# Performance work log

Hardware: AMD Instinct MI355X
Metric: run time of the kernel (lower is better)

Reference implementation:

```python
import jax, jax.numpy as jnp
import numpy as np

THRESH = 0.4


def setup_inputs() -> dict:
    key = jax.random.key(0)
    ks = jax.random.split(key, 8)
    B, N, C, H, O = 8, 16384, 640, 256, 128
    s = 0.02  # small init so sigmoid(logits) ~ 0.5 -> realistic mixed selection
    return {
        "point_features": jax.random.normal(ks[0], (B, N, C), jnp.float32),
        "point_coords": jax.random.normal(ks[1], (B, N, 3), jnp.float32) * 10.0,
        "w1": jax.random.normal(ks[2], (C, H), jnp.float32) * s,
        "b1": jnp.zeros((H,), jnp.float32),
        "w2": jax.random.normal(ks[3], (H, 1), jnp.float32) * s,
        "b2": jnp.zeros((1,), jnp.float32),
        "wo": jax.random.normal(ks[4], (C, O), jnp.float32) * s,
        "bo": jnp.zeros((O,), jnp.float32),
    }


def reference(point_features, point_coords, w1, b1, w2, b2, wo, bo):
    B, N, _ = point_features.shape
    # 2-layer MLP -> per-point logit -> sigmoid score
    h = jax.nn.relu(jnp.einsum('bnc,ch->bnh', point_features, w1) + b1)
    logits = jnp.einsum('bnh,ho->bno', h, w2) + b2          # [B, N, 1]
    scores = jax.nn.sigmoid(logits)                          # [B, N, 1]
    # score-scaled features through output projection
    feats = jnp.einsum('bnc,co->bno', point_features * scores, wo) + bo  # [B, N, O]
    # score-threshold selection + per-batch stream compaction into a
    # zero-padded tensor (padded to N, the jit-static worst case)
    sel = scores[..., 0] > THRESH                            # [B, N] bool
    pos = jnp.cumsum(sel.astype(jnp.int32), axis=1) - 1      # destination slot
    pos = jnp.where(sel, pos, N)                             # unselected -> OOB (dropped)
    bidx = jnp.arange(B)[:, None]
    selected_keypoints = jnp.zeros_like(feats).at[bidx, pos].set(feats, mode='drop')
    selected_coords = jnp.zeros_like(point_coords).at[bidx, pos].set(point_coords, mode='drop')
    # point_mask: True where the row is zero padding (matches (coords==0).sum(-1)!=0)
    point_mask = jnp.sum(selected_coords == 0, axis=-1) != 0
    return selected_keypoints, selected_coords, point_mask
```

## Files before the change

kernel.cpp:

```cpp
#include <hip/hip_runtime.h>
#include <hip/hip_bf16.h>


typedef __attribute__((ext_vector_type(8))) short short8v;
typedef __attribute__((ext_vector_type(4))) float f32x4;

#define M_TOTAL 131072
#define C_DIM 640
#define H_DIM 256
#define O_DIM 128
#define NCOMB 384
#define TM 64
#define KSTEPS 20
#define N_PTS 16384
#define TILES_PER_B 256
#define NTILES 2048
#define THRL -0.4054651081f
#define FIX_MARGIN 0.03f

#define OUT_COORD_OFF 16777216
#define OUT_MASK_OFF  17170432

#define WT_OFF     0u
#define TMASK_OFF  491520u
#define TAGG_OFF   507904u
#define TEXCL_OFF  516096u
#define COUNTS_OFF 524288u
#define G_OFF      1572864u

__device__ __forceinline__ int swzA(int u) {
  return u ^ (((u >> 3) & 1) | (((u >> 6) & 3) << 1));
}
__device__ __forceinline__ int swzB(int u) { return u ^ ((u >> 3) & 7); }

__device__ __forceinline__ void glds16(const void* g, void* l) {
  const __attribute__((address_space(1))) unsigned int* gp =
      reinterpret_cast<const __attribute__((address_space(1))) unsigned int*>(
          reinterpret_cast<uintptr_t>(g));
  __attribute__((address_space(3))) unsigned int* lp =
      reinterpret_cast<__attribute__((address_space(3))) unsigned int*>(
          reinterpret_cast<uintptr_t>(l));
  __builtin_amdgcn_global_load_lds(gp, lp, 16, 0, 0);
}

__device__ __forceinline__ unsigned int f2bf_bits(float f) {
  unsigned int u = __builtin_bit_cast(unsigned int, f);
  return (u + 0x7fffu + ((u >> 16) & 1u)) >> 16;
}
__device__ __forceinline__ unsigned int pack_bf2(float lo, float hi) {
  return f2bf_bits(lo) | (f2bf_bits(hi) << 16);
}

__global__ __launch_bounds__(256) void convert_w(const float* __restrict__ w1,
                                                 const float* __restrict__ wo,
                                                 unsigned short* __restrict__ Wt2) {
  int o = blockIdx.x * 256 + threadIdx.x;
  if (o < NCOMB * C_DIM) {
    int e = o & 7;
    int chunk = o >> 3;
    int ks = chunk / 1536;
    int r = chunk - ks * 1536;
    int u = swzB(r);
    int n = u >> 2, kg = u & 3;
    int k = ks * 32 + kg * 8 + e;
    float v = (n < H_DIM) ? w1[k * H_DIM + n] : wo[k * O_DIM + (n - H_DIM)];
    Wt2[o] = (unsigned short)f2bf_bits(v);
  }
}

__global__ __launch_bounds__(512, 4) void gemm_fused(
    const float* __restrict__ pf, const unsigned short* __restrict__ Wt2,
    const float* __restrict__ w1, const float* __restrict__ b1,
    const float* __restrict__ w2, const float* __restrict__ b2,
    const float* __restrict__ bo, unsigned long long* __restrict__ tmask,
    int* __restrict__ tagg, float* __restrict__ G) {
  __shared__ __align__(16) unsigned short As[2][256 * 8];
  __shared__ __align__(16) unsigned short Bs[2][1536 * 8];
  __shared__ float lpart[8][64];
  __shared__ float llog[64];
  __shared__ float srow[64];
  __shared__ unsigned long long s_fixmask;

  const int tid = threadIdx.x;
  const int lane = tid & 63;
  const int wv = tid >> 6;
  const int q = lane & 15;
  const int p = lane >> 4;
  const int tile = blockIdx.x;
  const int m0 = tile * TM;

  f32x4 acc[3][4];
#pragma unroll
  for (int i = 0; i < 3; ++i)
#pragma unroll
    for (int rt = 0; rt < 4; ++rt) acc[i][rt] = (f32x4){0.f, 0.f, 0.f, 0.f};

  const int ar = tid >> 3;
  const int ah = tid & 7;
  const float* asrc = pf + (size_t)(m0 + ar) * C_DIM + ah * 4;
  const int awp = swzA(((ah >> 1) << 6) + ar) * 8 + (ah & 1) * 4;

  float4 rB;
  {
    float4 rA = *(const float4*)(asrc);
    rB = *(const float4*)(asrc + 32);
#pragma unroll
    for (int u = 0; u < 3; ++u)
      glds16(Wt2 + (size_t)(u * 512 + tid) * 8, &Bs[0][(u * 512 + tid) * 8]);
    *(uint2*)&As[0][awp] = make_uint2(pack_bf2(rA.x, rA.y), pack_bf2(rA.z, rA.w));
    __syncthreads();
  }

#pragma unroll 2
  for (int t = 0; t < KSTEPS; ++t) {
    const int cur = t & 1;
    float4 rC;
    if (t + 2 < KSTEPS) rC = *(const float4*)(asrc + (t + 2) * 32);
    if (t + 1 < KSTEPS) {
#pragma unroll
      for (int u = 0; u < 3; ++u)
        glds16(Wt2 + (size_t)((t + 1) * 1536 + u * 512 + tid) * 8,
               &Bs[cur ^ 1][(u * 512 + tid) * 8]);
    }
    short8v af[4];
#pragma unroll
    for (int rt = 0; rt < 4; ++rt)
      af[rt] = *(const short8v*)&As[cur][swzA((p << 6) + rt * 16 + q) * 8];
#pragma unroll
    for (int i = 0; i < 3; ++i) {
      const int ub = (((wv + 8 * i) * 16 + q) << 2) + p;
      short8v bfv = *(const short8v*)&Bs[cur][swzB(ub) * 8];
#pragma unroll
      for (int rt = 0; rt < 4; ++rt)
        acc[i][rt] = __builtin_amdgcn_mfma_f32_16x16x32_bf16(af[rt], bfv, acc[i][rt], 0, 0, 0);
    }
    if (t + 1 < KSTEPS)
      *(uint2*)&As[cur ^ 1][awp] = make_uint2(pack_bf2(rB.x, rB.y), pack_bf2(rB.z, rB.w));
    rB = rC;
    __syncthreads();
  }

  float w2v[2], b1v[2];
#pragma unroll
  for (int i = 0; i < 2; ++i) {
    int col = (wv + 8 * i) * 16 + q;
    w2v[i] = w2[col];
    b1v[i] = b1[col];
  }
#pragma unroll
  for (int rt = 0; rt < 4; ++rt) {
    float pr[4] = {0.f, 0.f, 0.f, 0.f};
#pragma unroll
    for (int i = 0; i < 2; ++i)
#pragma unroll
      for (int r = 0; r < 4; ++r)
        pr[r] += fmaxf(acc[i][rt][r] + b1v[i], 0.f) * w2v[i];
#pragma unroll
    for (int mk = 1; mk < 16; mk <<= 1)
#pragma unroll
      for (int r = 0; r < 4; ++r) pr[r] += __shfl_xor(pr[r], mk);
    if (q == 0)
#pragma unroll
      for (int r = 0; r < 4; ++r) lpart[wv][rt * 16 + p * 4 + r] = pr[r];
  }
  __syncthreads();

  bool nf = false;
  if (wv == 0) {
    float lg = b2[0];
#pragma unroll
    for (int w = 0; w < 8; ++w) lg += lpart[w][tid];
    llog[tid] = lg;
    nf = fabsf(lg - THRL) < FIX_MARGIN;
  }
  unsigned long long fm = __ballot(nf);
  if (tid == 0) s_fixmask = fm;
  __syncthreads();

  unsigned long long fixmask = s_fixmask;
  while (fixmask) {
    int row = __ffsll(fixmask) - 1;
    fixmask &= fixmask - 1;
    if (tid < 256) {
      const float* prow = pf + (size_t)(m0 + row) * C_DIM;
      float a0 = 0.f, a1 = 0.f;
      for (int c = 0; c < C_DIM; c += 2) {
        a0 = fmaf(prow[c], w1[(size_t)c * H_DIM + tid], a0);
        a1 = fmaf(prow[c + 1], w1[(size_t)(c + 1) * H_DIM + tid], a1);
      }
      float v = fmaxf(a0 + a1 + b1[tid], 0.f) * w2[tid];
#pragma unroll
      for (int mk = 1; mk < 64; mk <<= 1) v += __shfl_xor(v, mk);
      if (lane == 0) lpart[0][wv] = v;
    }
    __syncthreads();
    if (tid == 0)
      llog[row] = lpart[0][0] + lpart[0][1] + lpart[0][2] + lpart[0][3] + b2[0];
    __syncthreads();
  }

  bool sel = false;
  float flog = 0.f;
  if (wv == 0) {
    flog = llog[tid];
    sel = flog > THRL;
  }
  unsigned long long selmask = __ballot(sel);
  if (wv == 0) {
    srow[tid] = 1.f / (1.f + expf(-flog));
    if (tid == 0) {
      tmask[tile] = selmask;
      tagg[tile] = __popcll(selmask);
    }
  }
  __syncthreads();

  {
    const int gcol = wv * 16 + q;
    const float bov = bo[gcol];
#pragma unroll
    for (int rt = 0; rt < 4; ++rt)
#pragma unroll
      for (int r = 0; r < 4; ++r) {
        int row = rt * 16 + p * 4 + r;
        G[(size_t)(m0 + row) * O_DIM + gcol] = fmaf(acc[2][rt][r], srow[row], bov);
      }
  }
}

__global__ __launch_bounds__(256) void scan_tiles(const int* __restrict__ tagg,
                                                  int* __restrict__ texcl,
                                                  int* __restrict__ counts) {
  __shared__ int wsum[4];
  const int c = blockIdx.x, t = threadIdx.x;
  const int lane = t & 63, w = t >> 6;
  int v = tagg[c * 256 + t];
  int inc = v;
#pragma unroll
  for (int d = 1; d < 64; d <<= 1) {
    int n = __shfl_up(inc, d);
    if (lane >= d) inc += n;
  }
  if (lane == 63) wsum[w] = inc;
  __syncthreads();
  int base = 0;
#pragma unroll
  for (int ww = 0; ww < 4; ++ww)
    if (ww < w) base += wsum[ww];
  texcl[c * 256 + t] = base + inc - v;
  if (t == 255) counts[c] = base + inc;
}

__global__ __launch_bounds__(512) void scatter(
    const float* __restrict__ G, const unsigned long long* __restrict__ tmask,
    const int* __restrict__ texcl, const float* __restrict__ pc,
    float* __restrict__ out) {
  const int tile = blockIdx.x;
  const int tid = threadIdx.x;
  const int lane = tid & 63;
  const int wv = tid >> 6;
  const unsigned long long mask = tmask[tile];
  const int base = (tile >> 8) * N_PTS + texcl[tile];
  const int m0 = tile * TM;
#pragma unroll
  for (int j = 0; j < 8; ++j) {
    const int row = wv * 8 + j;
    if (!((mask >> row) & 1ull)) continue;
    const int dst = base + __popcll(mask & ((1ull << row) - 1ull));
    const int m = m0 + row;
    float2 g = *(const float2*)(G + (size_t)m * O_DIM + lane * 2);
    *(float2*)(out + (size_t)dst * O_DIM + lane * 2) = g;
    if (lane == 0) {
      float c0 = pc[m * 3], c1 = pc[m * 3 + 1], c2 = pc[m * 3 + 2];
      float* oc = out + OUT_COORD_OFF;
      oc[dst * 3] = c0; oc[dst * 3 + 1] = c1; oc[dst * 3 + 2] = c2;
      out[OUT_MASK_OFF + dst] = (c0 == 0.f || c1 == 0.f || c2 == 0.f) ? 1.f : 0.f;
    }
  }
}

__global__ __launch_bounds__(256) void fill_tail(const int* __restrict__ counts,
                                                 float* __restrict__ out) {
  int m = blockIdx.x * 4 + (threadIdx.x >> 6);
  int lane = threadIdx.x & 63;
  int b = m >> 14, j = m & (N_PTS - 1);
  if (j < counts[b]) return;
  *(float2*)(out + (size_t)m * O_DIM + lane * 2) = make_float2(0.f, 0.f);
  if (lane == 0) {
    float* oc = out + OUT_COORD_OFF;
    oc[m * 3] = 0.f; oc[m * 3 + 1] = 0.f; oc[m * 3 + 2] = 0.f;
    out[OUT_MASK_OFF + m] = 1.f;
  }
}

extern "C" void kernel_launch(void* const* d_in, const int* in_sizes, int n_in,
                              void* d_out, int out_size, void* d_ws, size_t ws_size,
                              hipStream_t stream) {
  const float* pf = (const float*)d_in[0];
  const float* pc = (const float*)d_in[1];
  const float* w1 = (const float*)d_in[2];
  const float* b1 = (const float*)d_in[3];
  const float* w2 = (const float*)d_in[4];
  const float* b2 = (const float*)d_in[5];
  const float* wo = (const float*)d_in[6];
  const float* bo = (const float*)d_in[7];
  float* out = (float*)d_out;
  char* ws = (char*)d_ws;

  unsigned short* Wt2 = (unsigned short*)(ws + WT_OFF);
  unsigned long long* tmask = (unsigned long long*)(ws + TMASK_OFF);
  int* tagg = (int*)(ws + TAGG_OFF);
  int* texcl = (int*)(ws + TEXCL_OFF);
  int* counts = (int*)(ws + COUNTS_OFF);
  float* G = (float*)(ws + G_OFF);

  convert_w<<<960, 256, 0, stream>>>(w1, wo, Wt2);
  gemm_fused<<<NTILES, 512, 0, stream>>>(pf, Wt2, w1, b1, w2, b2, bo,
                                         tmask, tagg, G);
  scan_tiles<<<8, 256, 0, stream>>>(tagg, texcl, counts);
  scatter<<<NTILES, 512, 0, stream>>>(G, tmask, texcl, pc, out);
  fill_tail<<<M_TOTAL / 4, 256, 0, stream>>>(counts, out);
}
```

Measured before the change: 200.4 us.

## Double GEMM row tile to 128 with 2x4 warp layout for weight reuse

Grows the fused GEMM tile from 64 to 128 rows and reorganizes the 8 warps into 2 row groups by 4 column groups, each computing 6 column tiles. Each LDS-staged weight tile is reused across twice as many rows, which halves weight loads and barrier overhead per row. In exchange the accumulator count doubles, the occupancy hint drops from 4 to 3, and the tile count halves. The scan and scatter kernels are adapted to use two 64-bit selection masks per tile.

```diff
diff --git a/kernel.cpp b/kernel.cpp
--- a/kernel.cpp
+++ b/kernel.cpp
@@ -10,11 +10,11 @@
 #define H_DIM 256
 #define O_DIM 128
 #define NCOMB 384
-#define TM 64
+#define TM 128
 #define KSTEPS 20
 #define N_PTS 16384
-#define TILES_PER_B 256
-#define NTILES 2048
+#define TILES_PER_B 128
+#define NTILES 1024
 #define THRL -0.4054651081f
 #define FIX_MARGIN 0.03f
 
@@ -24,12 +24,12 @@
 #define WT_OFF     0u
 #define TMASK_OFF  491520u
 #define TAGG_OFF   507904u
-#define TEXCL_OFF  516096u
-#define COUNTS_OFF 524288u
+#define TEXCL_OFF  512000u
+#define COUNTS_OFF 516096u
 #define G_OFF      1572864u
 
-__device__ __forceinline__ int swzA(int u) {
-  return u ^ (((u >> 3) & 1) | (((u >> 6) & 3) << 1));
+__device__ __forceinline__ int swzA2(int u) {
+  return u ^ (((u >> 3) & 1) | (((u >> 7) & 3) << 1));
 }
 __device__ __forceinline__ int swzB(int u) { return u ^ ((u >> 3) & 7); }
 
@@ -68,54 +68,64 @@
   }
 }
 
-__global__ __launch_bounds__(512, 4) void gemm_fused(
+__global__ __launch_bounds__(512, 3) void gemm_fused(
     const float* __restrict__ pf, const unsigned short* __restrict__ Wt2,
     const float* __restrict__ w1, const float* __restrict__ b1,
     const float* __restrict__ w2, const float* __restrict__ b2,
     const float* __restrict__ bo, unsigned long long* __restrict__ tmask,
     int* __restrict__ tagg, float* __restrict__ G) {
-  __shared__ __align__(16) unsigned short As[2][256 * 8];
+  __shared__ __align__(16) unsigned short As[2][512 * 8];
   __shared__ __align__(16) unsigned short Bs[2][1536 * 8];
-  __shared__ float lpart[8][64];
-  __shared__ float llog[64];
-  __shared__ float srow[64];
-  __shared__ unsigned long long s_fixmask;
+  __shared__ float lpart[3][128];
+  __shared__ float llog[128];
+  __shared__ float srow[128];
+  __shared__ float fsum[4];
+  __shared__ unsigned long long s_fm[2];
+  __shared__ unsigned long long s_msk[2];
 
   const int tid = threadIdx.x;
   const int lane = tid & 63;
   const int wv = tid >> 6;
   const int q = lane & 15;
   const int p = lane >> 4;
+  const int wr = wv & 1;
+  const int wc = wv >> 1;
   const int tile = blockIdx.x;
   const int m0 = tile * TM;
 
-  f32x4 acc[3][4];
-#pragma unroll
-  for (int i = 0; i < 3; ++i)
+  f32x4 acc[6][4];
+#pragma unroll
+  for (int i = 0; i < 6; ++i)
 #pragma unroll
     for (int rt = 0; rt < 4; ++rt) acc[i][rt] = (f32x4){0.f, 0.f, 0.f, 0.f};
 
-  const int ar = tid >> 3;
-  const int ah = tid & 7;
-  const float* asrc = pf + (size_t)(m0 + ar) * C_DIM + ah * 4;
-  const int awp = swzA(((ah >> 1) << 6) + ar) * 8 + (ah & 1) * 4;
-
-  float4 rB;
+  const int arow = tid >> 2;
+  const int akg = tid & 3;
+  const float* asrc = pf + (size_t)(m0 + arow) * C_DIM + akg * 8;
+  const int awp = swzA2(akg * 128 + arow) * 8;
+
+  float4 rB0, rB1;
   {
-    float4 rA = *(const float4*)(asrc);
-    rB = *(const float4*)(asrc + 32);
+    float4 a0 = *(const float4*)(asrc);
+    float4 a1 = *(const float4*)(asrc + 4);
 #pragma unroll
     for (int u = 0; u < 3; ++u)
       glds16(Wt2 + (size_t)(u * 512 + tid) * 8, &Bs[0][(u * 512 + tid) * 8]);
-    *(uint2*)&As[0][awp] = make_uint2(pack_bf2(rA.x, rA.y), pack_bf2(rA.z, rA.w));
+    *(uint4*)&As[0][awp] = make_uint4(pack_bf2(a0.x, a0.y), pack_bf2(a0.z, a0.w),
+                                      pack_bf2(a1.x, a1.y), pack_bf2(a1.z, a1.w));
+    rB0 = *(const float4*)(asrc + 32);
+    rB1 = *(const float4*)(asrc + 36);
     __syncthreads();
   }
 
 #pragma unroll 2
   for (int t = 0; t < KSTEPS; ++t) {
     const int cur = t & 1;
-    float4 rC;
-    if (t + 2 < KSTEPS) rC = *(const float4*)(asrc + (t + 2) * 32);
+    float4 rC0 = rB0, rC1 = rB1;
+    if (t + 2 < KSTEPS) {
+      rC0 = *(const float4*)(asrc + (t + 2) * 32);
+      rC1 = *(const float4*)(asrc + (t + 2) * 32 + 4);
+    }
     if (t + 1 < KSTEPS) {
 #pragma unroll
       for (int u = 0; u < 3; ++u)
@@ -125,130 +135,142 @@
     short8v af[4];
 #pragma unroll
     for (int rt = 0; rt < 4; ++rt)
-      af[rt] = *(const short8v*)&As[cur][swzA((p << 6) + rt * 16 + q) * 8];
-#pragma unroll
-    for (int i = 0; i < 3; ++i) {
-      const int ub = (((wv + 8 * i) * 16 + q) << 2) + p;
+      af[rt] = *(const short8v*)&As[cur][swzA2(p * 128 + wr * 64 + rt * 16 + q) * 8];
+#pragma unroll
+    for (int i = 0; i < 6; ++i) {
+      const int ub = (((wc * 6 + i) * 16 + q) << 2) + p;
       short8v bfv = *(const short8v*)&Bs[cur][swzB(ub) * 8];
 #pragma unroll
       for (int rt = 0; rt < 4; ++rt)
         acc[i][rt] = __builtin_amdgcn_mfma_f32_16x16x32_bf16(af[rt], bfv, acc[i][rt], 0, 0, 0);
     }
     if (t + 1 < KSTEPS)
-      *(uint2*)&As[cur ^ 1][awp] = make_uint2(pack_bf2(rB.x, rB.y), pack_bf2(rB.z, rB.w));
-    rB = rC;
+      *(uint4*)&As[cur ^ 1][awp] = make_uint4(pack_bf2(rB0.x, rB0.y), pack_bf2(rB0.z, rB0.w),
+                                              pack_bf2(rB1.x, rB1.y), pack_bf2(rB1.z, rB1.w));
+    rB0 = rC0; rB1 = rC1;
     __syncthreads();
   }
 
-  float w2v[2], b1v[2];
-#pragma unroll
-  for (int i = 0; i < 2; ++i) {
-    int col = (wv + 8 * i) * 16 + q;
-    w2v[i] = w2[col];
-    b1v[i] = b1[col];
-  }
-#pragma unroll
-  for (int rt = 0; rt < 4; ++rt) {
-    float pr[4] = {0.f, 0.f, 0.f, 0.f};
-#pragma unroll
-    for (int i = 0; i < 2; ++i)
-#pragma unroll
-      for (int r = 0; r < 4; ++r)
-        pr[r] += fmaxf(acc[i][rt][r] + b1v[i], 0.f) * w2v[i];
-#pragma unroll
-    for (int mk = 1; mk < 16; mk <<= 1)
-#pragma unroll
-      for (int r = 0; r < 4; ++r) pr[r] += __shfl_xor(pr[r], mk);
-    if (q == 0)
-#pragma unroll
-      for (int r = 0; r < 4; ++r) lpart[wv][rt * 16 + p * 4 + r] = pr[r];
+  if (wc < 3) {
+    float b1v[6], w2v[6];
+#pragma unroll
+    for (int i = 0; i < 6; ++i) {
+      int ct = wc * 6 + i;
+      if (ct < 16) {
+        int col = ct * 16 + q;
+        b1v[i] = b1[col];
+        w2v[i] = w2[col];
+      } else {
+        b1v[i] = 0.f;
+        w2v[i] = 0.f;
+      }
+    }
+#pragma unroll
+    for (int rt = 0; rt < 4; ++rt) {
+      float pr[4] = {0.f, 0.f, 0.f, 0.f};
+#pragma unroll
+      for (int i = 0; i < 6; ++i) {
+        if (wc * 6 + i < 16) {
+#pragma unroll
+          for (int r = 0; r < 4; ++r)
+            pr[r] += fmaxf(acc[i][rt][r] + b1v[i], 0.f) * w2v[i];
+        }
+      }
+#pragma unroll
+      for (int mk = 1; mk < 16; mk <<= 1)
+#pragma unroll
+        for (int r = 0; r < 4; ++r) pr[r] += __shfl_xor(pr[r], mk);
+      if (q == 0)
+#pragma unroll
+        for (int r = 0; r < 4; ++r)
+          lpart[wc][wr * 64 + rt * 16 + p * 4 + r] = pr[r];
+    }
   }
   __syncthreads();
 
-  bool nf = false;
-  if (wv == 0) {
-    float lg = b2[0];
-#pragma unroll
-    for (int w = 0; w < 8; ++w) lg += lpart[w][tid];
+  if (tid < 128) {
+    float lg = lpart[0][tid] + lpart[1][tid] + lpart[2][tid] + b2[0];
     llog[tid] = lg;
-    nf = fabsf(lg - THRL) < FIX_MARGIN;
-  }
-  unsigned long long fm = __ballot(nf);
-  if (tid == 0) s_fixmask = fm;
+    bool nf = fabsf(lg - THRL) < FIX_MARGIN;
+    unsigned long long fm = __ballot(nf);
+    if (lane == 0) s_fm[wv] = fm;
+  }
   __syncthreads();
 
-  unsigned long long fixmask = s_fixmask;
-  while (fixmask) {
-    int row = __ffsll(fixmask) - 1;
-    fixmask &= fixmask - 1;
-    if (tid < 256) {
-      const float* prow = pf + (size_t)(m0 + row) * C_DIM;
-      float a0 = 0.f, a1 = 0.f;
-      for (int c = 0; c < C_DIM; c += 2) {
-        a0 = fmaf(prow[c], w1[(size_t)c * H_DIM + tid], a0);
-        a1 = fmaf(prow[c + 1], w1[(size_t)(c + 1) * H_DIM + tid], a1);
+#pragma unroll 1
+  for (int h = 0; h < 2; ++h) {
+    unsigned long long fixmask = s_fm[h];
+    while (fixmask) {
+      int row = h * 64 + (__ffsll(fixmask) - 1);
+      fixmask &= fixmask - 1;
+      if (tid < 256) {
+        const float* prow = pf + (size_t)(m0 + row) * C_DIM;
+        float a0 = 0.f, a1 = 0.f;
+        for (int c = 0; c < C_DIM; c += 2) {
+          a0 = fmaf(prow[c], w1[(size_t)c * H_DIM + tid], a0);
+          a1 = fmaf(prow[c + 1], w1[(size_t)(c + 1) * H_DIM + tid], a1);
+        }
+        float v = fmaxf(a0 + a1 + b1[tid], 0.f) * w2[tid];
+#pragma unroll
+        for (int mk = 1; mk < 64; mk <<= 1) v += __shfl_xor(v, mk);
+        if (lane == 0) fsum[wv] = v;
       }
-      float v = fmaxf(a0 + a1 + b1[tid], 0.f) * w2[tid];
-#pragma unroll
-      for (int mk = 1; mk < 64; mk <<= 1) v += __shfl_xor(v, mk);
-      if (lane == 0) lpart[0][wv] = v;
-    }
-    __syncthreads();
-    if (tid == 0)
-      llog[row] = lpart[0][0] + lpart[0][1] + lpart[0][2] + lpart[0][3] + b2[0];
-    __syncthreads();
-  }
-
-  bool sel = false;
-  float flog = 0.f;
-  if (wv == 0) {
-    flog = llog[tid];
-    sel = flog > THRL;
-  }
-  unsigned long long selmask = __ballot(sel);
-  if (wv == 0) {
+      __syncthreads();
+      if (tid == 0)
+        llog[row] = fsum[0] + fsum[1] + fsum[2] + fsum[3] + b2[0];
+      __syncthreads();
+    }
+  }
+
+  if (tid < 128) {
+    float flog = llog[tid];
+    bool sel = flog > THRL;
+    unsigned long long mk = __ballot(sel);
     srow[tid] = 1.f / (1.f + expf(-flog));
-    if (tid == 0) {
-      tmask[tile] = selmask;
-      tagg[tile] = __popcll(selmask);
-    }
+    if (lane == 0) s_msk[wv] = mk;
   }
   __syncthreads();
-
-  {
-    const int gcol = wv * 16 + q;
-    const float bov = bo[gcol];
-#pragma unroll
-    for (int rt = 0; rt < 4; ++rt)
-#pragma unroll
-      for (int r = 0; r < 4; ++r) {
-        int row = rt * 16 + p * 4 + r;
-        G[(size_t)(m0 + row) * O_DIM + gcol] = fmaf(acc[2][rt][r], srow[row], bov);
-      }
-  }
-}
-
-__global__ __launch_bounds__(256) void scan_tiles(const int* __restrict__ tagg,
+  if (tid == 0) {
+    tmask[2 * tile] = s_msk[0];
+    tmask[2 * tile + 1] = s_msk[1];
+    tagg[tile] = __popcll(s_msk[0]) + __popcll(s_msk[1]);
+  }
+
+#pragma unroll
+  for (int i = 0; i < 6; ++i) {
+    int ct = wc * 6 + i;
+    if (ct >= 16) {
+      int gcol = (ct - 16) * 16 + q;
+      float bov = bo[gcol];
+#pragma unroll
+      for (int rt = 0; rt < 4; ++rt)
+#pragma unroll
+        for (int r = 0; r < 4; ++r) {
+          int row = wr * 64 + rt * 16 + p * 4 + r;
+          G[(size_t)(m0 + row) * O_DIM + gcol] = fmaf(acc[i][rt][r], srow[row], bov);
+        }
+    }
+  }
+}
+
+__global__ __launch_bounds__(128) void scan_tiles(const int* __restrict__ tagg,
                                                   int* __restrict__ texcl,
                                                   int* __restrict__ counts) {
-  __shared__ int wsum[4];
+  __shared__ int ws0;
   const int c = blockIdx.x, t = threadIdx.x;
   const int lane = t & 63, w = t >> 6;
-  int v = tagg[c * 256 + t];
+  int v = tagg[c * 128 + t];
   int inc = v;
 #pragma unroll
   for (int d = 1; d < 64; d <<= 1) {
     int n = __shfl_up(inc, d);
     if (lane >= d) inc += n;
   }
-  if (lane == 63) wsum[w] = inc;
+  if (lane == 63 && w == 0) ws0 = inc;
   __syncthreads();
-  int base = 0;
-#pragma unroll
-  for (int ww = 0; ww < 4; ++ww)
-    if (ww < w) base += wsum[ww];
-  texcl[c * 256 + t] = base + inc - v;
-  if (t == 255) counts[c] = base + inc;
+  int base = (w == 1) ? ws0 : 0;
+  texcl[c * 128 + t] = base + inc - v;
+  if (t == 127) counts[c] = base + inc;
 }
 
 __global__ __launch_bounds__(512) void scatter(
@@ -259,22 +281,26 @@
   const int tid = threadIdx.x;
   const int lane = tid & 63;
   const int wv = tid >> 6;
-  const unsigned long long mask = tmask[tile];
-  const int base = (tile >> 8) * N_PTS + texcl[tile];
+  const unsigned long long mk0 = tmask[2 * tile];
+  const unsigned long long mk1 = tmask[2 * tile + 1];
+  const int c0 = __popcll(mk0);
+  const int base = (tile >> 7) * N_PTS + texcl[tile];
   const int m0 = tile * TM;
 #pragma unroll
-  for (int j = 0; j < 8; ++j) {
-    const int row = wv * 8 + j;
-    if (!((mask >> row) & 1ull)) continue;
-    const int dst = base + __popcll(mask & ((1ull << row) - 1ull));
+  for (int jj = 0; jj < 16; ++jj) {
+    const int row = wv * 16 + jj;
+    const unsigned long long mk = (row < 64) ? mk0 : mk1;
+    const int rb = row & 63;
+    if (!((mk >> rb) & 1ull)) continue;
+    const int dst = base + __popcll(mk & ((1ull << rb) - 1ull)) + ((row < 64) ? 0 : c0);
     const int m = m0 + row;
     float2 g = *(const float2*)(G + (size_t)m * O_DIM + lane * 2);
     *(float2*)(out + (size_t)dst * O_DIM + lane * 2) = g;
     if (lane == 0) {
-      float c0 = pc[m * 3], c1 = pc[m * 3 + 1], c2 = pc[m * 3 + 2];
+      float cx = pc[m * 3], cy = pc[m * 3 + 1], cz = pc[m * 3 + 2];
       float* oc = out + OUT_COORD_OFF;
-      oc[dst * 3] = c0; oc[dst * 3 + 1] = c1; oc[dst * 3 + 2] = c2;
-      out[OUT_MASK_OFF + dst] = (c0 == 0.f || c1 == 0.f || c2 == 0.f) ? 1.f : 0.f;
+      oc[dst * 3] = cx; oc[dst * 3 + 1] = cy; oc[dst * 3 + 2] = cz;
+      out[OUT_MASK_OFF + dst] = (cx == 0.f || cy == 0.f || cz == 0.f) ? 1.f : 0.f;
     }
   }
 }
@@ -317,7 +343,7 @@
   convert_w<<<960, 256, 0, stream>>>(w1, wo, Wt2);
   gemm_fused<<<NTILES, 512, 0, stream>>>(pf, Wt2, w1, b1, w2, b2, bo,
                                          tmask, tagg, G);
-  scan_tiles<<<8, 256, 0, stream>>>(tagg, texcl, counts);
+  scan_tiles<<<8, 128, 0, stream>>>(tagg, texcl, counts);
   scatter<<<NTILES, 512, 0, stream>>>(G, tmask, texcl, pc, out);
   fill_tail<<<M_TOTAL / 4, 256, 0, stream>>>(counts, out);
 }
```

Result: no change. 197.2 us (-1.6%).

## Triple-buffer weight tiles with explicit vmcnt waits and single barrier per K-step

Applied to the files above, without the earlier changes.

Switches the B (weight) LDS staging from double to triple buffering, issuing global_load_lds two steps ahead. The per-step __syncthreads is replaced by explicit s_waitcnt vmcnt/lgkmcnt plus one s_barrier, and the MFMA section is wrapped in s_setprio. The A-tile swizzle is simplified, and the epilogue scratch arrays now alias the GEMM LDS buffers so the larger B buffer stays within the LDS budget. The aim is to hide load latency and cut barrier stalls. The risks are more LDS per block, which may lower occupancy from the launch bound of 4, and fragile hand-written wait counts.

```diff
diff --git a/kernel.cpp b/kernel.cpp
--- a/kernel.cpp
+++ b/kernel.cpp
@@ -28,9 +28,9 @@
 #define COUNTS_OFF 524288u
 #define G_OFF      1572864u
 
-__device__ __forceinline__ int swzA(int u) {
-  return u ^ (((u >> 3) & 1) | (((u >> 6) & 3) << 1));
-}
+#define VMCNT(n) asm volatile("s_waitcnt vmcnt(" #n ")" ::: "memory")
+#define LGKMCNT0 asm volatile("s_waitcnt lgkmcnt(0)" ::: "memory")
+
 __device__ __forceinline__ int swzB(int u) { return u ^ ((u >> 3) & 7); }
 
 __device__ __forceinline__ void glds16(const void* g, void* l) {
@@ -74,12 +74,8 @@
     const float* __restrict__ w2, const float* __restrict__ b2,
     const float* __restrict__ bo, unsigned long long* __restrict__ tmask,
     int* __restrict__ tagg, float* __restrict__ G) {
-  __shared__ __align__(16) unsigned short As[2][256 * 8];
-  __shared__ __align__(16) unsigned short Bs[2][1536 * 8];
-  __shared__ float lpart[8][64];
-  __shared__ float llog[64];
-  __shared__ float srow[64];
-  __shared__ unsigned long long s_fixmask;
+  __shared__ __align__(16) unsigned short As[2][2048];
+  __shared__ __align__(16) unsigned short Bs[3][12288];
 
   const int tid = threadIdx.x;
   const int lane = tid & 63;
@@ -95,50 +91,65 @@
 #pragma unroll
     for (int rt = 0; rt < 4; ++rt) acc[i][rt] = (f32x4){0.f, 0.f, 0.f, 0.f};
 
-  const int ar = tid >> 3;
-  const int ah = tid & 7;
-  const float* asrc = pf + (size_t)(m0 + ar) * C_DIM + ah * 4;
-  const int awp = swzA(((ah >> 1) << 6) + ar) * 8 + (ah & 1) * 4;
-
-  float4 rB;
+  const float* asrc = pf + (size_t)(m0 + (tid >> 3)) * C_DIM + (tid & 7) * 4;
+  const int aphys = ((tid >> 1) ^ ((tid >> 4) & 3)) * 8 + (tid & 1) * 4;
+  const int aswz = (q >> 1) & 3;
+
+  float4 Rcur, Rnext;
   {
-    float4 rA = *(const float4*)(asrc);
-    rB = *(const float4*)(asrc + 32);
+    Rcur = *(const float4*)(asrc);
 #pragma unroll
     for (int u = 0; u < 3; ++u)
       glds16(Wt2 + (size_t)(u * 512 + tid) * 8, &Bs[0][(u * 512 + tid) * 8]);
-    *(uint2*)&As[0][awp] = make_uint2(pack_bf2(rA.x, rA.y), pack_bf2(rA.z, rA.w));
-    __syncthreads();
-  }
-
-#pragma unroll 2
+    Rnext = *(const float4*)(asrc + 32);
+#pragma unroll
+    for (int u = 0; u < 3; ++u)
+      glds16(Wt2 + (size_t)(1536 + u * 512 + tid) * 8, &Bs[1][(u * 512 + tid) * 8]);
+    *(uint2*)&As[0][aphys] = make_uint2(pack_bf2(Rcur.x, Rcur.y), pack_bf2(Rcur.z, Rcur.w));
+    Rcur = Rnext;
+  }
+
+#pragma unroll
   for (int t = 0; t < KSTEPS; ++t) {
-    const int cur = t & 1;
-    float4 rC;
-    if (t + 2 < KSTEPS) rC = *(const float4*)(asrc + (t + 2) * 32);
+    if (t < KSTEPS - 1) { VMCNT(4); } else { VMCNT(0); }
+    LGKMCNT0;
+    __builtin_amdgcn_s_barrier();
+    __builtin_amdgcn_sched_barrier(0);
+    if (t + 2 < KSTEPS) {
+      Rnext = *(const float4*)(asrc + (t + 2) * 32);
+#pragma unroll
+      for (int u = 0; u < 3; ++u)
+        glds16(Wt2 + (size_t)((t + 2) * 1536 + u * 512 + tid) * 8,
+               &Bs[(t + 2) % 3][(u * 512 + tid) * 8]);
+      __builtin_amdgcn_sched_barrier(0);
+    }
     if (t + 1 < KSTEPS) {
-#pragma unroll
-      for (int u = 0; u < 3; ++u)
-        glds16(Wt2 + (size_t)((t + 1) * 1536 + u * 512 + tid) * 8,
-               &Bs[cur ^ 1][(u * 512 + tid) * 8]);
+      *(uint2*)&As[(t + 1) & 1][aphys] =
+          make_uint2(pack_bf2(Rcur.x, Rcur.y), pack_bf2(Rcur.z, Rcur.w));
+      Rcur = Rnext;
     }
     short8v af[4];
 #pragma unroll
     for (int rt = 0; rt < 4; ++rt)
-      af[rt] = *(const short8v*)&As[cur][swzA((p << 6) + rt * 16 + q) * 8];
+      af[rt] = *(const short8v*)&As[t & 1][((rt * 64 + q * 4 + p) ^ aswz) * 8];
+    __builtin_amdgcn_s_setprio(1);
 #pragma unroll
     for (int i = 0; i < 3; ++i) {
       const int ub = (((wv + 8 * i) * 16 + q) << 2) + p;
-      short8v bfv = *(const short8v*)&Bs[cur][swzB(ub) * 8];
+      short8v bfv = *(const short8v*)&Bs[t % 3][swzB(ub) * 8];
 #pragma unroll
       for (int rt = 0; rt < 4; ++rt)
         acc[i][rt] = __builtin_amdgcn_mfma_f32_16x16x32_bf16(af[rt], bfv, acc[i][rt], 0, 0, 0);
     }
-    if (t + 1 < KSTEPS)
-      *(uint2*)&As[cur ^ 1][awp] = make_uint2(pack_bf2(rB.x, rB.y), pack_bf2(rB.z, rB.w));
-    rB = rC;
-    __syncthreads();
-  }
+    __builtin_amdgcn_s_setprio(0);
+  }
+  __syncthreads();
+
+  float* lpart = (float*)&As[0][0];
+  float* llog = (float*)&Bs[0][0];
+  float* srow = llog + 64;
+  float* fsum = srow + 64;
+  unsigned long long* s_fixmask = (unsigned long long*)(fsum + 4);
 
   float w2v[2], b1v[2];
 #pragma unroll
@@ -161,7 +172,7 @@
       for (int r = 0; r < 4; ++r) pr[r] += __shfl_xor(pr[r], mk);
     if (q == 0)
 #pragma unroll
-      for (int r = 0; r < 4; ++r) lpart[wv][rt * 16 + p * 4 + r] = pr[r];
+      for (int r = 0; r < 4; ++r) lpart[wv * 64 + rt * 16 + p * 4 + r] = pr[r];
   }
   __syncthreads();
 
@@ -169,15 +180,15 @@
   if (wv == 0) {
     float lg = b2[0];
 #pragma unroll
-    for (int w = 0; w < 8; ++w) lg += lpart[w][tid];
+    for (int w = 0; w < 8; ++w) lg += lpart[w * 64 + tid];
     llog[tid] = lg;
     nf = fabsf(lg - THRL) < FIX_MARGIN;
   }
   unsigned long long fm = __ballot(nf);
-  if (tid == 0) s_fixmask = fm;
-  __syncthreads();
-
-  unsigned long long fixmask = s_fixmask;
+  if (tid == 0) *s_fixmask = fm;
+  __syncthreads();
+
+  unsigned long long fixmask = *s_fixmask;
   while (fixmask) {
     int row = __ffsll(fixmask) - 1;
     fixmask &= fixmask - 1;
@@ -191,11 +202,11 @@
       float v = fmaxf(a0 + a1 + b1[tid], 0.f) * w2[tid];
 #pragma unroll
       for (int mk = 1; mk < 64; mk <<= 1) v += __shfl_xor(v, mk);
-      if (lane == 0) lpart[0][wv] = v;
+      if (lane == 0) fsum[wv] = v;
     }
     __syncthreads();
     if (tid == 0)
-      llog[row] = lpart[0][0] + lpart[0][1] + lpart[0][2] + lpart[0][3] + b2[0];
+      llog[row] = fsum[0] + fsum[1] + fsum[2] + fsum[3] + b2[0];
     __syncthreads();
   }
 
```

Result: no change. 197.4 us (-1.5%).
